# Performance work log

Hardware: AMD Instinct MI355X
Metric: run time of the kernel (lower is better)

Reference implementation:

```python
import jax, jax.numpy as jnp
import numpy as np

B, S, H, NH = 2, 2048, 4096, 32
D = H // NH  # head_dim = 128
ROPE_THETA = 10000.0


def setup_inputs() -> dict:
    key = jax.random.key(0)
    k0, k1, k2 = jax.random.split(key, 3)
    hidden_states = jax.random.normal(k0, (B, S, H), dtype=jnp.float32) * 0.02
    w_pack = jax.random.normal(k1, (H, 3 * H), dtype=jnp.float32) * 0.02  # fused QKV weight
    w_o = jax.random.normal(k2, (H, H), dtype=jnp.float32) * 0.02         # o_proj weight
    positions = jnp.broadcast_to(jnp.arange(S, dtype=jnp.int32), (B, S))
    return {"positions": positions, "hidden_states": hidden_states, "w_pack": w_pack, "w_o": w_o}


def _rope(x, positions):
    # neox-style rotary embedding (vLLM get_rope default), x: [B, S, NH, D]
    half = D // 2
    inv_freq = 1.0 / (ROPE_THETA ** (jnp.arange(0, half, dtype=jnp.float32) * 2.0 / D))
    freqs = positions.astype(jnp.float32)[..., None] * inv_freq  # [B, S, half]
    cos = jnp.cos(freqs)[:, :, None, :]  # [B, S, 1, half]
    sin = jnp.sin(freqs)[:, :, None, :]
    x1, x2 = x[..., :half], x[..., half:]
    return jnp.concatenate([x1 * cos - x2 * sin, x2 * cos + x1 * sin], axis=-1)


def reference(positions, hidden_states, w_pack, w_o):
    # fused QKV projection
    qkv = jnp.einsum('bsh,hf->bsf', hidden_states, w_pack)
    q, k, v = jnp.split(qkv, 3, axis=-1)
    q = q.reshape(B, S, NH, D)
    k = k.reshape(B, S, NH, D)
    v = v.reshape(B, S, NH, D)
    # RoPE on q, k
    q = _rope(q, positions)
    k = _rope(k, positions)
    # causal scaled dot-product attention
    scale = D ** -0.5
    scores = jnp.einsum('bqhd,bkhd->bhqk', q, k) * scale  # [B, NH, S, S]
    causal = jnp.tril(jnp.ones((S, S), dtype=bool))
    scores = jnp.where(causal[None, None], scores, jnp.finfo(scores.dtype).min)
    probs = jax.nn.softmax(scores, axis=-1)
    out = jnp.einsum('bhqk,bkhd->bqhd', probs, v).reshape(B, S, H)
    # output projection
    return jnp.einsum('bsh,hf->bsf', out, w_o)
```

## Files before the change

### kernel.cpp

```cpp
#include <hip/hip_runtime.h>

#define Sdim   2048
#define Hdim   4096
#define NHEADS 32
#define Dh     128
#define Mrows  4096
#define QKVLD  12288

typedef __attribute__((ext_vector_type(8))) short short8;
typedef __attribute__((ext_vector_type(4))) float f32x4;
typedef __attribute__((ext_vector_type(4))) float float4v;

__device__ __forceinline__ short f2bf(float f) {
  union { float f; unsigned u; } x; x.f = f;
  unsigned r = x.u + 0x7fffu + ((x.u >> 16) & 1u);
  return (short)(r >> 16);
}
__device__ __forceinline__ float bf2f(short s) {
  union { unsigned u; float f; } x; x.u = ((unsigned)(unsigned short)s) << 16;
  return x.f;
}

__device__ __forceinline__ void gload_lds16(const void* g, void* l) {
  __builtin_amdgcn_global_load_lds(
      (const __attribute__((address_space(1))) void*)g,
      (__attribute__((address_space(3))) void*)l, 16, 0, 0);
}

__global__ void k_cvt(const float* __restrict__ src, short* __restrict__ dst, int n8) {
  int idx = blockIdx.x * blockDim.x + threadIdx.x;
  if (idx >= n8) return;
  const float4v* s = (const float4v*)src + (size_t)idx * 2;
  float4v a = s[0], b = s[1];
  short8 o;
  o[0] = f2bf(a.x); o[1] = f2bf(a.y); o[2] = f2bf(a.z); o[3] = f2bf(a.w);
  o[4] = f2bf(b.x); o[5] = f2bf(b.y); o[6] = f2bf(b.z); o[7] = f2bf(b.w);
  *((short8*)dst + idx) = o;
}

__global__ void k_tcvt64(const float* __restrict__ src, short* __restrict__ dst,
                         int R, int C) {
  __shared__ float t[64][65];
  const int tid = threadIdx.x;
  const int r0 = blockIdx.y * 64, c0 = blockIdx.x * 64;
  const int ir = tid >> 4, ic = (tid & 15) << 2;
#pragma unroll
  for (int p = 0; p < 4; ++p) {
    const float4v v = *(const float4v*)(src + (size_t)(r0 + p * 16 + ir) * C + c0 + ic);
    t[p * 16 + ir][ic] = v.x; t[p * 16 + ir][ic + 1] = v.y;
    t[p * 16 + ir][ic + 2] = v.z; t[p * 16 + ir][ic + 3] = v.w;
  }
  __syncthreads();
  const int oc = tid >> 3, orr = (tid & 7) << 3;
#pragma unroll
  for (int p = 0; p < 2; ++p) {
    int c = p * 32 + oc;
    short8 o;
#pragma unroll
    for (int j = 0; j < 8; ++j) o[j] = f2bf(t[orr + j][c]);
    *(short8*)(dst + (size_t)(c0 + c) * R + r0 + orr) = o;
  }
}

__global__ void k_vt(const short* __restrict__ qkv, short* __restrict__ vt) {
  __shared__ short tile[32][33];
  int tx = threadIdx.x, ty = threadIdx.y;
  int hc0 = blockIdx.x * 32;
  int s0  = blockIdx.y * 32;
  int b   = blockIdx.z;
#pragma unroll
  for (int j = 0; j < 32; j += 8)
    tile[ty + j][tx] = qkv[(size_t)(b * 2048 + s0 + ty + j) * QKVLD + 8192 + hc0 + tx];
  __syncthreads();
#pragma unroll
  for (int j = 0; j < 32; j += 8)
    vt[(size_t)(b * 4096 + hc0 + ty + j) * Sdim + s0 + tx] = tile[tx][ty + j];
}

__device__ __forceinline__ void stage_half256(const short* G, int ld, int row0, int kcol,
                                              char* lds, int tid) {
#pragma unroll
  for (int j = 0; j < 2; ++j) {
    int p = j * 512 + tid;
    int r = p >> 3;
    int c = ((p & 7) ^ (r & 7)) << 3;
    gload_lds16(G + (size_t)(row0 + r) * ld + kcol + c,
                lds + ((j * 512 + (tid & 448)) << 4));
  }
}

#define MFMA_Q(qm, qn)                                                                   \
  do {                                                                                   \
    __builtin_amdgcn_s_setprio(1);                                                       \
    _Pragma("unroll")                                                                    \
    for (int m4 = 0; m4 < 4; ++m4)                                                       \
      _Pragma("unroll")                                                                  \
      for (int n2 = 0; n2 < 2; ++n2) {                                                   \
        acc[(qm)*4+m4][(qn)*2+n2] = __builtin_amdgcn_mfma_f32_16x16x32_bf16(             \
            av[m4][0], bv[(qn)*2+n2][0], acc[(qm)*4+m4][(qn)*2+n2], 0, 0, 0);            \
        acc[(qm)*4+m4][(qn)*2+n2] = __builtin_amdgcn_mfma_f32_16x16x32_bf16(             \
            av[m4][1], bv[(qn)*2+n2][1], acc[(qm)*4+m4][(qn)*2+n2], 0, 0, 0);            \
      }                                                                                  \
    __builtin_amdgcn_s_setprio(0);                                                       \
  } while (0)

#define PH_BARRIER()                    \
  do {                                  \
    __builtin_amdgcn_s_barrier();       \
    __builtin_amdgcn_sched_barrier(0);  \
  } while (0)

template<bool C_F32>
__global__ __launch_bounds__(512, 2) void k_gemm256(const short* __restrict__ A, int lda,
                                                    const short* __restrict__ Bt, int ldb,
                                                    void* __restrict__ Cp, int ldc,
                                                    int Ndim, int Kdim) {
  __shared__ __align__(16) char smem[131072];
  const int tid  = threadIdx.x;
  const int lane = tid & 63;
  const int wave = tid >> 6;
  const int lo = lane & 15, hi = lane >> 4;
  const int wr = wave >> 2, wc = wave & 3;

  const int nblk = gridDim.x;
  const int lid = (blockIdx.x & 7) * (nblk >> 3) + (blockIdx.x >> 3);
  const int nbn = Ndim >> 8;
  const int bm0 = (lid / nbn) << 8;
  const int bn0 = (lid % nbn) << 8;

  f32x4 acc[8][4];
#pragma unroll
  for (int i = 0; i < 8; ++i)
#pragma unroll
    for (int j = 0; j < 4; ++j) acc[i][j] = (f32x4){0.f, 0.f, 0.f, 0.f};

  short8 av[4][2], bv[4][2];
  const int swz = (lo & 7) << 4;
  const int brow = (wc & 1) * 64;

  stage_half256(Bt, ldb, bn0,       0, smem + 32768,         tid);
  stage_half256(Bt, ldb, bn0 + 128, 0, smem + 32768 + 16384, tid);
  stage_half256(A,  lda, bm0,       0, smem,                 tid);
  stage_half256(A,  lda, bm0 + 128, 0, smem + 16384,         tid);

  const int NK = Kdim >> 6;
  for (int kt = 0; kt < NK; ++kt) {
    const int cur = kt & 1;
    const char* Ab = smem + cur * 65536 + wr * 16384;
    const char* Bb = smem + cur * 65536 + 32768 + (wc >> 1) * 16384;
    char* nA = smem + (cur ^ 1) * 65536;
    char* nB = nA + 32768;
    const int kc = (kt + 1) << 6;
    const bool pf = (kt + 1 < NK);

    if (pf) {
      stage_half256(Bt, ldb, bn0,       kc, nB,         tid);
      stage_half256(Bt, ldb, bn0 + 128, kc, nB + 16384, tid);
      asm volatile("s_waitcnt vmcnt(4)" ::: "memory");
    } else {
      asm volatile("s_waitcnt vmcnt(0)" ::: "memory");
    }
    PH_BARRIER();
#pragma unroll
    for (int m4 = 0; m4 < 4; ++m4)
#pragma unroll
      for (int ks = 0; ks < 2; ++ks)
        av[m4][ks] = *(const short8*)(Ab + (m4 * 16 + lo) * 128 + ((ks * 64 + hi * 16) ^ swz));
#pragma unroll
    for (int ni = 0; ni < 2; ++ni)
#pragma unroll
      for (int ks = 0; ks < 2; ++ks)
        bv[ni][ks] = *(const short8*)(Bb + (brow + ni * 16 + lo) * 128 + ((ks * 64 + hi * 16) ^ swz));
    MFMA_Q(0, 0);
#pragma unroll
    for (int ni = 2; ni < 4; ++ni)
#pragma unroll
      for (int ks = 0; ks < 2; ++ks)
        bv[ni][ks] = *(const short8*)(Bb + (brow + ni * 16 + lo) * 128 + ((ks * 64 + hi * 16) ^ swz));

    if (pf) {
      stage_half256(A, lda, bm0,       kc, nA,         tid);
      stage_half256(A, lda, bm0 + 128, kc, nA + 16384, tid);
    }
    PH_BARRIER();
    MFMA_Q(0, 1);
#pragma unroll
    for (int m4 = 0; m4 < 4; ++m4)
#pragma unroll
      for (int ks = 0; ks < 2; ++ks)
        av[m4][ks] = *(const short8*)(Ab + ((64 + m4 * 16 + lo) * 128) + ((ks * 64 + hi * 16) ^ swz));

    PH_BARRIER();
    MFMA_Q(1, 0);

    PH_BARRIER();
    MFMA_Q(1, 1);
  }

#pragma unroll
  for (int mi = 0; mi < 8; ++mi)
#pragma unroll
    for (int r = 0; r < 4; ++r) {
      int row = bm0 + wr * 128 + mi * 16 + hi * 4 + r;
#pragma unroll
      for (int ni = 0; ni < 4; ++ni) {
        int col = bn0 + wc * 64 + ni * 16 + lo;
        if (C_F32) ((float*)Cp)[(size_t)row * ldc + col] = acc[mi][ni][r];
        else       ((short*)Cp)[(size_t)row * ldc + col] = f2bf(acc[mi][ni][r]);
      }
    }
}

__global__ void k_rope8(short* qkv, const int* __restrict__ positions) {
  int idx = blockIdx.x * 256 + threadIdx.x;
  int t = idx & 7;
  int h = (idx >> 3) & 31;
  int row = idx >> 8;
  float pos = (float)positions[row];
  size_t o = (size_t)row * QKVLD + h * 128 + t * 8;
  short8 q1 = *(short8*)(qkv + o),        q2 = *(short8*)(qkv + o + 64);
  short8 k1 = *(short8*)(qkv + o + 4096), k2 = *(short8*)(qkv + o + 4160);
#pragma unroll
  for (int j = 0; j < 8; ++j) {
    int d = t * 8 + j;
    float inv = exp2f((float)d * -0.2076205059304570f);
    float ang = pos * inv, s, c;
    sincosf(ang, &s, &c);
    float a1 = bf2f(q1[j]), a2 = bf2f(q2[j]);
    q1[j] = f2bf(a1 * c - a2 * s); q2[j] = f2bf(a2 * c + a1 * s);
    float b1 = bf2f(k1[j]), b2 = bf2f(k2[j]);
    k1[j] = f2bf(b1 * c - b2 * s); k2[j] = f2bf(b2 * c + b1 * s);
  }
  *(short8*)(qkv + o) = q1;        *(short8*)(qkv + o + 64) = q2;
  *(short8*)(qkv + o + 4096) = k1; *(short8*)(qkv + o + 4160) = k2;
}

__device__ __forceinline__ void stage_kv(const short* Kb, const short* Vtb, int kv0,
                                         char* kbuf, char* vbuf, int tid, int wave) {
#pragma unroll
  for (int i = 0; i < 4; ++i) {
    int p = i * 256 + tid;
    int r = p >> 4;
    int c = (p & 15) ^ (r & 7);
    gload_lds16(Kb + (size_t)(kv0 + r) * QKVLD + (c << 3),
                kbuf + ((i * 256 + wave * 64) << 4));
  }
#pragma unroll
  for (int i = 0; i < 4; ++i) {
    int p = i * 256 + tid;
    int r = p >> 3;
    int c = (p & 7) ^ (r & 7);
    gload_lds16(Vtb + (size_t)r * Sdim + kv0 + (c << 3),
                vbuf + ((i * 256 + wave * 64) << 4));
  }
}

__global__ __launch_bounds__(256, 2) void k_attn(short* __restrict__ qkv,
                                                 const short* __restrict__ Vt) {
  __shared__ __align__(16) char smem[81920];
  const int tid  = threadIdx.x;
  const int lane = tid & 63;
  const int wave = tid >> 6;
  const int lo = lane & 15, hi = lane >> 4;

  const int bid = blockIdx.x;
  const int lid = (bid & 7) * 128 + (bid >> 3);
  const int bh = lid >> 4;
  const int qt = 15 - (lid & 15);
  const int b = bh >> 5, h = bh & 31;
  const int q0 = qt << 7;

  short* base = qkv + (size_t)b * Sdim * QKVLD;
  const short* Qb = base + h * Dh;
  const short* Kb = base + Hdim + h * Dh;
  const short* Vtb = Vt + (size_t)(b * 32 + h) * 128 * Sdim;
  const int qrow0 = q0 + wave * 32;

  short* Pw = (short*)(smem + 65536 + wave * 4096);

  short8 qf[2][4];
#pragma unroll
  for (int mi = 0; mi < 2; ++mi)
#pragma unroll
    for (int ks = 0; ks < 4; ++ks)
      qf[mi][ks] = *(const short8*)(Qb + (size_t)(qrow0 + mi * 16 + lo) * QKVLD + ks * 32 + hi * 8);

  f32x4 acc_o[2][9];
  float m_run[2][4];
#pragma unroll
  for (int mi = 0; mi < 2; ++mi) {
#pragma unroll
    for (int nf = 0; nf < 9; ++nf) acc_o[mi][nf] = (f32x4){0.f, 0.f, 0.f, 0.f};
#pragma unroll
    for (int r = 0; r < 4; ++r) m_run[mi][r] = -1e30f;
  }

  short8 vones;
#pragma unroll
  for (int j = 0; j < 8; ++j) vones[j] = (short)0x3F80;

  const float SEXP = 0.088388347648318447f * 1.4426950408889634f;
  const int nkv = (q0 + 128) >> 6;
  const int swz = (lo & 7) << 4;

  stage_kv(Kb, Vtb, 0, smem, smem + 16384, tid, wave);
  __syncthreads();

  int cur = 0;
  for (int kvt = 0; kvt < nkv; ++kvt) {
    const int kv0 = kvt << 6;
    if (kvt + 1 < nkv)
      stage_kv(Kb, Vtb, kv0 + 64, smem + (cur ^ 1) * 32768,
               smem + (cur ^ 1) * 32768 + 16384, tid, wave);

    if (kv0 <= qrow0 + 31) {
      const char* kl = smem + cur * 32768;
      const char* vl = smem + cur * 32768 + 16384;

      f32x4 accs[2][4];
#pragma unroll
      for (int mi = 0; mi < 2; ++mi)
#pragma unroll
        for (int nf = 0; nf < 4; ++nf) accs[mi][nf] = (f32x4){0.f, 0.f, 0.f, 0.f};
#pragma unroll
      for (int ks = 0; ks < 4; ++ks) {
        short8 kf[4];
#pragma unroll
        for (int nf = 0; nf < 4; ++nf) {
          int r = nf * 16 + lo;
          kf[nf] = *(const short8*)(kl + r * 256 + ((ks * 64 + hi * 16) ^ swz));
        }
        __builtin_amdgcn_s_setprio(1);
#pragma unroll
        for (int mi = 0; mi < 2; ++mi)
#pragma unroll
          for (int nf = 0; nf < 4; ++nf)
            accs[mi][nf] = __builtin_amdgcn_mfma_f32_16x16x32_bf16(qf[mi][ks], kf[nf], accs[mi][nf], 0, 0, 0);
        __builtin_amdgcn_s_setprio(0);
      }

      const bool needmask = (kv0 + 63 > qrow0);
      float pmax[2][4];
      bool okall = true;
#pragma unroll
      for (int mi = 0; mi < 2; ++mi) {
#pragma unroll
        for (int r = 0; r < 4; ++r) {
          const int qrow = qrow0 + mi * 16 + hi * 4 + r;
          float tmax = -1e30f;
#pragma unroll
          for (int nf = 0; nf < 4; ++nf) {
            float v = accs[mi][nf][r] * SEXP;
            if (needmask) {
              int col = kv0 + nf * 16 + lo;
              v = (col <= qrow) ? v : -1e30f;
            }
            accs[mi][nf][r] = v;
            tmax = fmaxf(tmax, v);
          }
#pragma unroll
          for (int off = 1; off < 16; off <<= 1)
            tmax = fmaxf(tmax, __shfl_xor(tmax, off, 64));
          pmax[mi][r] = tmax;
          okall = okall && (tmax <= m_run[mi][r] + 8.0f);
        }
      }
      if (!__all(okall)) {
#pragma unroll
        for (int mi = 0; mi < 2; ++mi)
#pragma unroll
          for (int r = 0; r < 4; ++r) {
            float mnew = fmaxf(m_run[mi][r], pmax[mi][r]);
            float alpha = exp2f(m_run[mi][r] - mnew);
            m_run[mi][r] = mnew;
#pragma unroll
            for (int nf = 0; nf < 9; ++nf) acc_o[mi][nf][r] *= alpha;
          }
      }
#pragma unroll
      for (int mi = 0; mi < 2; ++mi)
#pragma unroll
        for (int r = 0; r < 4; ++r) {
          const int prow = mi * 16 + hi * 4 + r;
          const int psw = prow & 7;
#pragma unroll
          for (int nf = 0; nf < 4; ++nf) {
            float p = exp2f(accs[mi][nf][r] - m_run[mi][r]);
            int col = nf * 16 + lo;
            Pw[(prow << 6) + (((col >> 3) ^ psw) << 3) + (col & 7)] = f2bf(p);
          }
        }

#pragma unroll
      for (int ks = 0; ks < 2; ++ks) {
        short8 pf[2];
#pragma unroll
        for (int mi = 0; mi < 2; ++mi) {
          int prow = mi * 16 + lo;
          pf[mi] = *(const short8*)((const char*)Pw + prow * 128 + (((ks * 4 + hi) ^ (prow & 7)) << 4));
        }
        __builtin_amdgcn_s_setprio(1);
#pragma unroll
        for (int nf = 0; nf < 9; ++nf) {
          short8 vf;
          if (nf < 8) {
            int row = nf * 16 + lo;
            vf = *(const short8*)(vl + row * 128 + ((ks * 64 + hi * 16) ^ swz));
          } else {
            vf = vones;
          }
#pragma unroll
          for (int mi = 0; mi < 2; ++mi)
            acc_o[mi][nf] = __builtin_amdgcn_mfma_f32_16x16x32_bf16(pf[mi], vf, acc_o[mi][nf], 0, 0, 0);
        }
        __builtin_amdgcn_s_setprio(0);
      }
    }

    __syncthreads();
    cur ^= 1;
  }

  short* Osm = (short*)smem;
#pragma unroll
  for (int mi = 0; mi < 2; ++mi)
#pragma unroll
    for (int r = 0; r < 4; ++r) {
      float inv = 1.0f / acc_o[mi][8][r];
      int row = wave * 32 + mi * 16 + hi * 4 + r;
#pragma unroll
      for (int nf = 0; nf < 8; ++nf)
        Osm[row * 128 + nf * 16 + lo] = f2bf(acc_o[mi][nf][r] * inv);
    }
  __syncthreads();
  short* Ob = base + h * Dh;
#pragma unroll
  for (int it = 0; it < 8; ++it) {
    int chunk = it * 256 + tid;
    int row = chunk >> 4, c8 = chunk & 15;
    *(short8*)(Ob + (size_t)(q0 + row) * QKVLD + c8 * 8) =
        *(const short8*)(Osm + row * 128 + c8 * 8);
  }
}

extern "C" void kernel_launch(void* const* d_in, const int* in_sizes, int n_in,
                              void* d_out, int out_size, void* d_ws, size_t ws_size,
                              hipStream_t stream) {
  const int*   positions = (const int*)d_in[0];
  const float* hidden    = (const float*)d_in[1];
  const float* w_pack    = (const float*)d_in[2];
  const float* w_o       = (const float*)d_in[3];
  float* out = (float*)d_out;

  char* ws = (char*)d_ws;
  short* Wpt  = (short*)ws;
  short* qkvb = (short*)(ws + (size_t)12288 * 4096 * 2);
  short* Wot  = (short*)ws;
  short* Hbf  = (short*)d_out;
  short* Vtg  = (short*)((char*)d_out + ((size_t)32 << 20));

  k_cvt<<<8192, 256, 0, stream>>>(hidden, Hbf, 4096 * 4096 / 8);
  k_tcvt64<<<dim3(12288 / 64, 4096 / 64), 256, 0, stream>>>(w_pack, Wpt, 4096, 12288);
  k_gemm256<false><<<dim3(768), 512, 0, stream>>>(Hbf, 4096, Wpt, 4096, qkvb, QKVLD, 12288, 4096);
  k_rope8<<<4096, 256, 0, stream>>>(qkvb, positions);
  k_vt<<<dim3(128, 64, 2), dim3(32, 8), 0, stream>>>(qkvb, Vtg);
  k_attn<<<dim3(1024), 256, 0, stream>>>(qkvb, Vtg);
  k_tcvt64<<<dim3(4096 / 64, 4096 / 64), 256, 0, stream>>>(w_o, Wot, 4096, 4096);
  k_gemm256<true><<<dim3(256), 512, 0, stream>>>(qkvb, QKVLD, Wot, 4096, out, 4096, 4096, 4096);
}
```

Measured before the change: 766.5 us.

## Fuse RoPE and V transpose into QKV GEMM epilogue via LDS staging

```diff
diff --git a/kernel.cpp b/kernel.cpp
--- a/kernel.cpp
+++ b/kernel.cpp
@@ -60,21 +60,6 @@
     for (int j = 0; j < 8; ++j) o[j] = f2bf(t[orr + j][c]);
     *(short8*)(dst + (size_t)(c0 + c) * R + r0 + orr) = o;
   }
-}
-
-__global__ void k_vt(const short* __restrict__ qkv, short* __restrict__ vt) {
-  __shared__ short tile[32][33];
-  int tx = threadIdx.x, ty = threadIdx.y;
-  int hc0 = blockIdx.x * 32;
-  int s0  = blockIdx.y * 32;
-  int b   = blockIdx.z;
-#pragma unroll
-  for (int j = 0; j < 32; j += 8)
-    tile[ty + j][tx] = qkv[(size_t)(b * 2048 + s0 + ty + j) * QKVLD + 8192 + hc0 + tx];
-  __syncthreads();
-#pragma unroll
-  for (int j = 0; j < 32; j += 8)
-    vt[(size_t)(b * 4096 + hc0 + ty + j) * Sdim + s0 + tx] = tile[tx][ty + j];
 }
 
 __device__ __forceinline__ void stage_half256(const short* G, int ld, int row0, int kcol,
@@ -110,11 +95,17 @@
     __builtin_amdgcn_sched_barrier(0);  \
   } while (0)
 
-template<bool C_F32>
+__device__ __forceinline__ int ct_addr(int row, int col) {
+  return row * 512 + ((((col >> 3) ^ ((row >> 3) & 7)) << 4) | ((col & 7) << 1));
+}
+
+template<int MODE>
 __global__ __launch_bounds__(512, 2) void k_gemm256(const short* __restrict__ A, int lda,
                                                     const short* __restrict__ Bt, int ldb,
                                                     void* __restrict__ Cp, int ldc,
-                                                    int Ndim, int Kdim) {
+                                                    int Ndim, int Kdim,
+                                                    const int* __restrict__ positions,
+                                                    short* __restrict__ Vtg) {
   __shared__ __align__(16) char smem[131072];
   const int tid  = threadIdx.x;
   const int lane = tid & 63;
@@ -197,42 +188,95 @@
     MFMA_Q(1, 1);
   }
 
-#pragma unroll
-  for (int mi = 0; mi < 8; ++mi)
-#pragma unroll
-    for (int r = 0; r < 4; ++r) {
-      int row = bm0 + wr * 128 + mi * 16 + hi * 4 + r;
-#pragma unroll
-      for (int ni = 0; ni < 4; ++ni) {
-        int col = bn0 + wc * 64 + ni * 16 + lo;
-        if (C_F32) ((float*)Cp)[(size_t)row * ldc + col] = acc[mi][ni][r];
-        else       ((short*)Cp)[(size_t)row * ldc + col] = f2bf(acc[mi][ni][r]);
+  if (MODE == 0) {
+#pragma unroll
+    for (int mi = 0; mi < 8; ++mi)
+#pragma unroll
+      for (int r = 0; r < 4; ++r) {
+        int row = bm0 + wr * 128 + mi * 16 + hi * 4 + r;
+#pragma unroll
+        for (int ni = 0; ni < 4; ++ni) {
+          int col = bn0 + wc * 64 + ni * 16 + lo;
+          ((float*)Cp)[(size_t)row * ldc + col] = acc[mi][ni][r];
+        }
+      }
+  } else {
+    PH_BARRIER();
+    short* Ct = (short*)smem;
+#pragma unroll
+    for (int mi = 0; mi < 8; ++mi)
+#pragma unroll
+      for (int r = 0; r < 4; ++r) {
+        int row = wr * 128 + mi * 16 + hi * 4 + r;
+#pragma unroll
+        for (int ni = 0; ni < 4; ++ni) {
+          int col = wc * 64 + ni * 16 + lo;
+          *(short*)((char*)Ct + ct_addr(row, col)) = f2bf(acc[mi][ni][r]);
+        }
+      }
+    PH_BARRIER();
+
+    short* qkvb = (short*)Cp;
+    if (bn0 < 8192) {
+#pragma unroll
+      for (int it = 0; it < 16; ++it) {
+        int idx = it * 512 + tid;
+        int row = idx >> 5, c8 = idx & 31;
+        int col0 = c8 * 8;
+        int dloc = (bn0 + col0) & 127;
+        float pos = (float)positions[bm0 + row];
+        short8 o;
+        if (dloc < 64) {
+#pragma unroll
+          for (int j = 0; j < 8; ++j) {
+            int d = dloc + j;
+            float inv = exp2f((float)d * -0.2076205059304570f);
+            float s, c; sincosf(pos * inv, &s, &c);
+            float x1 = bf2f(*(const short*)((const char*)Ct + ct_addr(row, col0 + j)));
+            float x2 = bf2f(*(const short*)((const char*)Ct + ct_addr(row, col0 + j + 64)));
+            o[j] = f2bf(x1 * c - x2 * s);
+          }
+        } else {
+#pragma unroll
+          for (int j = 0; j < 8; ++j) {
+            int d = dloc - 64 + j;
+            float inv = exp2f((float)d * -0.2076205059304570f);
+            float s, c; sincosf(pos * inv, &s, &c);
+            float x2 = bf2f(*(const short*)((const char*)Ct + ct_addr(row, col0 + j)));
+            float x1 = bf2f(*(const short*)((const char*)Ct + ct_addr(row, col0 + j - 64)));
+            o[j] = f2bf(x2 * c + x1 * s);
+          }
+        }
+        *(short8*)(qkvb + (size_t)(bm0 + row) * QKVLD + bn0 + col0) = o;
+      }
+    } else {
+#pragma unroll
+      for (int it = 0; it < 16; ++it) {
+        int idx = it * 512 + tid;
+        int row = idx >> 5, c8 = idx & 31;
+        int col0 = c8 * 8;
+        short8 o;
+#pragma unroll
+        for (int j = 0; j < 8; ++j)
+          o[j] = *(const short*)((const char*)Ct + ct_addr(row, col0 + j));
+        *(short8*)(qkvb + (size_t)(bm0 + row) * QKVLD + bn0 + col0) = o;
+      }
+      const int b = bm0 >> 11, srow0 = bm0 & 2047;
+#pragma unroll
+      for (int it = 0; it < 16; ++it) {
+        int idx = it * 512 + tid;
+        int vcol = idx >> 5;
+        int s8 = (idx & 31) << 3;
+        int gcolv = bn0 - 8192 + vcol;
+        int h = gcolv >> 7, d = gcolv & 127;
+        short8 o;
+#pragma unroll
+        for (int j = 0; j < 8; ++j)
+          o[j] = *(const short*)((const char*)Ct + ct_addr(s8 + j, vcol));
+        *(short8*)(Vtg + (size_t)((b * 32 + h) * 128 + d) * Sdim + srow0 + s8) = o;
       }
     }
-}
-
-__global__ void k_rope8(short* qkv, const int* __restrict__ positions) {
-  int idx = blockIdx.x * 256 + threadIdx.x;
-  int t = idx & 7;
-  int h = (idx >> 3) & 31;
-  int row = idx >> 8;
-  float pos = (float)positions[row];
-  size_t o = (size_t)row * QKVLD + h * 128 + t * 8;
-  short8 q1 = *(short8*)(qkv + o),        q2 = *(short8*)(qkv + o + 64);
-  short8 k1 = *(short8*)(qkv + o + 4096), k2 = *(short8*)(qkv + o + 4160);
-#pragma unroll
-  for (int j = 0; j < 8; ++j) {
-    int d = t * 8 + j;
-    float inv = exp2f((float)d * -0.2076205059304570f);
-    float ang = pos * inv, s, c;
-    sincosf(ang, &s, &c);
-    float a1 = bf2f(q1[j]), a2 = bf2f(q2[j]);
-    q1[j] = f2bf(a1 * c - a2 * s); q2[j] = f2bf(a2 * c + a1 * s);
-    float b1 = bf2f(k1[j]), b2 = bf2f(k2[j]);
-    k1[j] = f2bf(b1 * c - b2 * s); k2[j] = f2bf(b2 * c + b1 * s);
-  }
-  *(short8*)(qkv + o) = q1;        *(short8*)(qkv + o + 64) = q2;
-  *(short8*)(qkv + o + 4096) = k1; *(short8*)(qkv + o + 4160) = k2;
+  }
 }
 
 __device__ __forceinline__ void stage_kv(const short* Kb, const short* Vtb, int kv0,
@@ -461,10 +505,10 @@
 
   k_cvt<<<8192, 256, 0, stream>>>(hidden, Hbf, 4096 * 4096 / 8);
   k_tcvt64<<<dim3(12288 / 64, 4096 / 64), 256, 0, stream>>>(w_pack, Wpt, 4096, 12288);
-  k_gemm256<false><<<dim3(768), 512, 0, stream>>>(Hbf, 4096, Wpt, 4096, qkvb, QKVLD, 12288, 4096);
-  k_rope8<<<4096, 256, 0, stream>>>(qkvb, positions);
-  k_vt<<<dim3(128, 64, 2), dim3(32, 8), 0, stream>>>(qkvb, Vtg);
+  k_gemm256<1><<<dim3(768), 512, 0, stream>>>(Hbf, 4096, Wpt, 4096, qkvb, QKVLD, 12288, 4096,
+                                              positions, Vtg);
   k_attn<<<dim3(1024), 256, 0, stream>>>(qkvb, Vtg);
   k_tcvt64<<<dim3(4096 / 64, 4096 / 64), 256, 0, stream>>>(w_o, Wot, 4096, 4096);
-  k_gemm256<true><<<dim3(256), 512, 0, stream>>>(qkvb, QKVLD, Wot, 4096, out, 4096, 4096, 4096);
-}
+  k_gemm256<0><<<dim3(256), 512, 0, stream>>>(qkvb, QKVLD, Wot, 4096, out, 4096, 4096, 4096,
+                                              nullptr, nullptr);
+}
```

Result: slower. 789.8 us (+3.0%).
